# Kernel optimization log

Hardware: AMD Instinct MI355X
Metric: run time of the kernel (lower is better)

## Reference

```python
import jax, jax.numpy as jnp
import numpy as np

N = 40000          # nodes
E = 640000         # edges
D_IN, D_HID, D_EMB, D_OUT = 128, 128, 64, 2


def glorot(key, shape):
    lim = np.sqrt(6.0 / (shape[0] + shape[1]))
    return jax.random.uniform(key, shape, jnp.float32, -lim, lim)


def setup_inputs() -> dict:
    key = jax.random.key(0)
    ks = jax.random.split(key, 8)
    x = jax.random.normal(ks[0], (N, D_IN), jnp.float32)
    edge_index = jax.random.randint(ks[1], (2, E), 0, N, dtype=jnp.int64)
    # GCNConv weights stored as [in, out]; biases zero-init per PyG default
    W1 = glorot(ks[2], (D_IN, D_HID));  b1 = jnp.zeros((D_HID,), jnp.float32)
    W2 = glorot(ks[3], (D_HID, D_HID)); b2 = jnp.zeros((D_HID,), jnp.float32)
    W3 = glorot(ks[4], (D_HID, D_EMB)); b3 = jnp.zeros((D_EMB,), jnp.float32)
    Wout = glorot(ks[5], (D_EMB, D_OUT)); bout = jnp.zeros((D_OUT,), jnp.float32)
    return {"x": x, "edge_index": edge_index,
            "W1": W1, "b1": b1, "W2": W2, "b2": b2,
            "W3": W3, "b3": b3, "Wout": Wout, "bout": bout}


def _gcn_norm(edge_index, n):
    # add self loops, compute symmetric normalization d^-1/2[src] * d^-1/2[dst]
    loop = jnp.arange(n, dtype=edge_index.dtype)
    src = jnp.concatenate([edge_index[0], loop])
    dst = jnp.concatenate([edge_index[1], loop])
    deg = jax.ops.segment_sum(jnp.ones_like(dst, dtype=jnp.float32), dst,
                              num_segments=n)
    dinv = jax.lax.rsqrt(deg)                      # deg >= 1 due to self-loops
    dinv = jnp.where(jnp.isinf(dinv), 0.0, dinv)
    return src, dst, dinv[src] * dinv[dst]


def gcn_conv(x, src, dst, norm, W, b):
    h = x @ W                                      # [N, out]
    msg = h[src] * norm[:, None]                   # gather + scale  [E+N, out]
    return jax.ops.segment_sum(msg, dst, num_segments=x.shape[0]) + b


def reference(x, edge_index, W1, b1, W2, b2, W3, b3, Wout, bout):
    n = x.shape[0]
    src, dst, norm = _gcn_norm(edge_index, n)      # cached=True: computed once
    h = jax.nn.relu(gcn_conv(x, src, dst, norm, W1, b1))   # dropout is identity in eval
    h = jax.nn.relu(gcn_conv(h, src, dst, norm, W2, b2))
    h = gcn_conv(h, src, dst, norm, W3, b3)
    out = h @ Wout + bout
    return (out, h)
```

## Files before the change

### kernel.cpp

```cpp
#include <hip/hip_runtime.h>
#include <hip/hip_bf16.h>

#define NN 40000
#define NE 640000

typedef unsigned int u32;
typedef unsigned short u16;
typedef __attribute__((ext_vector_type(8))) short bf16x8;
typedef __attribute__((ext_vector_type(4))) float f32x4;

__device__ float g_wf[512];
__device__ u16   g_wp[40960];
__device__ int   g_flags[4];
__device__ int   g_cnt[NN];
__device__ int   g_cur[NN];
__device__ int   g_rowptr[NN + 1];
__device__ float g_dinv[NN];
__device__ int   g_csrc[NE];
__device__ int   g_bsum[64];
__device__ u16   g_ha[(size_t)NN * 128];
__device__ u16   g_hb[(size_t)NN * 128];

#define OFF_B1 0
#define OFF_B2 128
#define OFF_B3 256
#define OFF_WO 320
#define OFF_BO 448
#define WP_W1 0
#define WP_W2 16384
#define WP_W3 32768

__device__ __forceinline__ float b2f(u16 v){ return __uint_as_float(((u32)v) << 16); }
__device__ __forceinline__ float blo(u32 u){ return __uint_as_float(u << 16); }
__device__ __forceinline__ float bhi(u32 u){ return __uint_as_float(u & 0xffff0000u); }
__device__ __forceinline__ u32 f2bf(float f){
  u32 u = __float_as_uint(f);
  return (u + 0x7fffu + ((u >> 16) & 1u)) >> 16;
}
__device__ __forceinline__ int clampi(int v, int lo, int hi){ return v < lo ? lo : (v > hi ? hi : v); }
__device__ __forceinline__ u16 ldbf(const void* p, int idx){
  return g_flags[0] ? (u16)f2bf(((const float*)p)[idx]) : ((const u16*)p)[idx];
}
__device__ __forceinline__ float ldf(const void* p, int idx){
  return g_flags[0] ? ((const float*)p)[idx] : b2f(((const u16*)p)[idx]);
}

__global__ __launch_bounds__(256) void k_detect(const u16* __restrict__ xf, const int* __restrict__ ei){
  __shared__ int c1, c2;
  if (threadIdx.x == 0){ c1 = 0; c2 = 0; }
  __syncthreads();
  int l1 = 0, l2 = 0;
  for (int i = threadIdx.x; i < 4096; i += 256){
    u16 v = xf[2 * i];
    int e = (v >> 7) & 0xff;
    if (v == 0 || (e >= 100 && e <= 140)) l1++;
    if (ei[2 * i + 1] == 0) l2++;
  }
  atomicAdd(&c1, l1); atomicAdd(&c2, l2);
  __syncthreads();
  if (threadIdx.x == 0){
    g_flags[0] = (c1 < 2048) ? 1 : 0;
    g_flags[1] = (c2 > 2048) ? 2 : 1;
  }
}

__global__ __launch_bounds__(256) void k_prep(const void* xin, const void* w1, const void* b1,
                                              const void* w2, const void* b2, const void* w3,
                                              const void* b3, const void* wo, const void* bo){
  int T = (int)blockIdx.x * 256 + (int)threadIdx.x;
  if (T < 640000){
    if (g_flags[0]){
      const float4* p = (const float4*)xin + (size_t)T * 2;
      float4 a = p[0], b = p[1];
      uint4 o;
      o.x = f2bf(a.x) | (f2bf(a.y) << 16);
      o.y = f2bf(a.z) | (f2bf(a.w) << 16);
      o.z = f2bf(b.x) | (f2bf(b.y) << 16);
      o.w = f2bf(b.z) | (f2bf(b.w) << 16);
      ((uint4*)g_ha)[T] = o;
    } else {
      ((uint4*)g_ha)[T] = ((const uint4*)xin)[T];
    }
  } else if (T < 680960){
    int local = T - 640000;
    int J, dstbase, l; const void* src;
    if (local < 16384){ J = 128; src = w1; dstbase = WP_W1; l = local; }
    else if (local < 32768){ J = 128; src = w2; dstbase = WP_W2; l = local - 16384; }
    else { J = 64; src = w3; dstbase = WP_W3; l = local - 32768; }
    int chunk = l >> 9, within = l & 511;
    int nbw = J / 16;
    int kb = chunk / nbw, nb = chunk % nbw;
    int lane = within >> 3, j = within & 7;
    int q = lane >> 4, n = lane & 15;
    int k = kb * 32 + q * 8 + j;
    int col = nb * 16 + n;
    g_wp[dstbase + l] = ldbf(src, k * J + col);
  } else if (T < 681410){
    int l = T - 680960;
    if (l < 128)      g_wf[OFF_B1 + l] = ldf(b1, l);
    else if (l < 256) g_wf[OFF_B2 + l - 128] = ldf(b2, l - 128);
    else if (l < 320) g_wf[OFF_B3 + l - 256] = ldf(b3, l - 256);
    else if (l < 448) g_wf[OFF_WO + l - 320] = ldf(wo, l - 320);
    else              g_wf[OFF_BO + l - 448] = ldf(bo, l - 448);
  } else if (T < 721410){
    g_cnt[T - 681410] = 0;
  } else if (T < 761450){
    g_cur[T - 721410] = 0;
  }
}

__global__ __launch_bounds__(256) void k_count(const int* __restrict__ ei){
  int e = blockIdx.x * 256 + threadIdx.x;
  if (e < NE){
    int strd = g_flags[1];
    int d = clampi(ei[(size_t)(NE + e) * strd], 0, NN - 1);
    atomicAdd(&g_cnt[d], 1);
  }
}

__global__ __launch_bounds__(1024) void k_scan1(){
  int t = (int)threadIdx.x;
  int b = (int)blockIdx.x;
  int i = b * 1024 + t;
  int v = (i < NN) ? g_cnt[i] : 0;
  int lane = t & 63, wv = t >> 6;
  int x = v;
#pragma unroll
  for (int ofs = 1; ofs < 64; ofs <<= 1){
    int y = __shfl_up(x, ofs, 64);
    if (lane >= ofs) x += y;
  }
  __shared__ int wsum[16];
  if (lane == 63) wsum[wv] = x;
  __syncthreads();
  if (t < 16){
    int s = wsum[t];
#pragma unroll
    for (int ofs = 1; ofs < 16; ofs <<= 1){
      int y = __shfl_up(s, ofs, 64);
      if (t >= ofs) s += y;
    }
    wsum[t] = s;
  }
  __syncthreads();
  int pre = (wv == 0) ? 0 : wsum[wv - 1];
  int incl = x + pre;
  if (i < NN){
    g_rowptr[i] = incl - v;
    g_dinv[i] = rsqrtf((float)(v + 1));
  }
  if (t == 1023) g_bsum[b] = incl;
}

__global__ __launch_bounds__(1024) void k_scan3(){
  __shared__ int pre;
  int t = (int)threadIdx.x;
  if (t < 64){
    int v = (t < 40) ? g_bsum[t] : 0;
    int s = v;
#pragma unroll
    for (int ofs = 1; ofs < 64; ofs <<= 1){
      int y = __shfl_up(s, ofs, 64);
      if (t >= ofs) s += y;
    }
    if (t == (int)blockIdx.x) pre = s - v;
    if (blockIdx.x == 0 && t == 39) g_rowptr[NN] = s;
  }
  __syncthreads();
  int i = (int)blockIdx.x * 1024 + t;
  if (i < NN) g_rowptr[i] += pre;
}

__global__ __launch_bounds__(256) void k_fill(const int* __restrict__ ei){
  int part = (int)blockIdx.x & 7;
  int chunk = (int)blockIdx.x >> 3;
  int lo = part * 5000, hi = lo + 5000;
  int strd = g_flags[1];
  int tid = (int)threadIdx.x;
#pragma unroll
  for (int it = 0; it < 8; ++it){
    int e = chunk * 2048 + it * 256 + tid;
    if (e < NE){
      int d = clampi(ei[(size_t)(NE + e) * strd], 0, NN - 1);
      if (d >= lo && d < hi){
        int s = clampi(ei[(size_t)e * strd], 0, NN - 1);
        int pos = clampi(g_rowptr[d] + atomicAdd(&g_cur[d], 1), 0, NE - 1);
        g_csrc[pos] = s;
      }
    }
  }
}

template<int J>
__global__ __launch_bounds__(256) void k_gemm(int wpoff){
  constexpr int NB = J / 16;
  int tid = (int)threadIdx.x;
  int wave = tid >> 6, lane = tid & 63;
  int q = lane >> 4, n = lane & 15;
  int m0 = (int)blockIdx.x * 64 + wave * 16;
  f32x4 acc[NB];
#pragma unroll
  for (int nb = 0; nb < NB; ++nb) acc[nb] = (f32x4){0.f, 0.f, 0.f, 0.f};
  const u16* arow = g_ha + (size_t)(m0 + n) * 128 + q * 8;
#pragma unroll
  for (int kb = 0; kb < 4; ++kb){
    bf16x8 a = *(const bf16x8*)(arow + kb * 32);
    const u16* wbase = g_wp + wpoff + (kb * NB) * 512 + lane * 8;
#pragma unroll
    for (int nb = 0; nb < NB; ++nb){
      bf16x8 w = *(const bf16x8*)(wbase + nb * 512);
      acc[nb] = __builtin_amdgcn_mfma_f32_16x16x32_bf16(a, w, acc[nb], 0, 0, 0);
    }
  }
  u16* crow = g_hb + (size_t)(m0 + q * 4) * J + n;
#pragma unroll
  for (int r = 0; r < 4; ++r){
    float di = g_dinv[m0 + q * 4 + r];
#pragma unroll
    for (int nb = 0; nb < NB; ++nb)
      crow[(size_t)r * J + nb * 16] = (u16)f2bf(acc[nb][r] * di);
  }
}

#define ACC8(P) do { \
    a0 += blo((P).x); a1 += bhi((P).x); \
    a2 += blo((P).y); a3 += bhi((P).y); \
    a4 += blo((P).z); a5 += bhi((P).z); \
    a6 += blo((P).w); a7 += bhi((P).w); } while (0)

template<int J, bool RELU>
__global__ __launch_bounds__(256, 4) void k_agg(int boff, float* __restrict__ h3, float* __restrict__ outp){
  constexpr int LPR = J / 8;
  int gt = (int)blockIdx.x * 256 + (int)threadIdx.x;
  int wid = gt / LPR;
  int lane = (int)threadIdx.x & (LPR - 1);
  if (wid >= NN) return;
  int cc = lane * 8;
  const u16* __restrict__ hb = g_hb;
  float di = g_dinv[wid];
  int beg = g_rowptr[wid], end = g_rowptr[wid + 1];
  uint4 ps = *(const uint4*)(hb + (size_t)wid * J + cc);
  float a0 = 0.f, a1 = 0.f, a2 = 0.f, a3 = 0.f, a4 = 0.f, a5 = 0.f, a6 = 0.f, a7 = 0.f;
  for (int e = beg; e < end; e += 8){
    int s0, s1, s2, s3, s4, s5, s6, s7;
    {
      int last = end - 1;
#define LDS_IDX(T) clampi(g_csrc[(e + T < last) ? (e + T) : last], 0, NN - 1)
      s0 = LDS_IDX(0); s1 = LDS_IDX(1); s2 = LDS_IDX(2); s3 = LDS_IDX(3);
      s4 = LDS_IDX(4); s5 = LDS_IDX(5); s6 = LDS_IDX(6); s7 = LDS_IDX(7);
#undef LDS_IDX
    }
    uint4 p0 = *(const uint4*)(hb + (size_t)s0 * J + cc);
    uint4 p1 = *(const uint4*)(hb + (size_t)s1 * J + cc);
    uint4 p2 = *(const uint4*)(hb + (size_t)s2 * J + cc);
    uint4 p3 = *(const uint4*)(hb + (size_t)s3 * J + cc);
    uint4 p4 = *(const uint4*)(hb + (size_t)s4 * J + cc);
    uint4 p5 = *(const uint4*)(hb + (size_t)s5 * J + cc);
    uint4 p6 = *(const uint4*)(hb + (size_t)s6 * J + cc);
    uint4 p7 = *(const uint4*)(hb + (size_t)s7 * J + cc);
    int nv = end - e;
    ACC8(p0);
    if (nv > 1) ACC8(p1);
    if (nv > 2) ACC8(p2);
    if (nv > 3) ACC8(p3);
    if (nv > 4) ACC8(p4);
    if (nv > 5) ACC8(p5);
    if (nv > 6) ACC8(p6);
    if (nv > 7) ACC8(p7);
  }
  ACC8(ps);
  a0 = a0 * di + g_wf[boff + cc];
  a1 = a1 * di + g_wf[boff + cc + 1];
  a2 = a2 * di + g_wf[boff + cc + 2];
  a3 = a3 * di + g_wf[boff + cc + 3];
  a4 = a4 * di + g_wf[boff + cc + 4];
  a5 = a5 * di + g_wf[boff + cc + 5];
  a6 = a6 * di + g_wf[boff + cc + 6];
  a7 = a7 * di + g_wf[boff + cc + 7];
  if (RELU){
    a0 = fmaxf(a0, 0.f); a1 = fmaxf(a1, 0.f); a2 = fmaxf(a2, 0.f); a3 = fmaxf(a3, 0.f);
    a4 = fmaxf(a4, 0.f); a5 = fmaxf(a5, 0.f); a6 = fmaxf(a6, 0.f); a7 = fmaxf(a7, 0.f);
  }
  if (J == 128){
    uint4 o;
    o.x = f2bf(a0) | (f2bf(a1) << 16);
    o.y = f2bf(a2) | (f2bf(a3) << 16);
    o.z = f2bf(a4) | (f2bf(a5) << 16);
    o.w = f2bf(a6) | (f2bf(a7) << 16);
    *(uint4*)(g_ha + (size_t)wid * 128 + cc) = o;
  } else {
    *(float4*)(h3 + (size_t)wid * 64 + cc)     = make_float4(a0, a1, a2, a3);
    *(float4*)(h3 + (size_t)wid * 64 + cc + 4) = make_float4(a4, a5, a6, a7);
    float o0 = a0 * g_wf[OFF_WO + (cc + 0) * 2] + a1 * g_wf[OFF_WO + (cc + 1) * 2]
             + a2 * g_wf[OFF_WO + (cc + 2) * 2] + a3 * g_wf[OFF_WO + (cc + 3) * 2]
             + a4 * g_wf[OFF_WO + (cc + 4) * 2] + a5 * g_wf[OFF_WO + (cc + 5) * 2]
             + a6 * g_wf[OFF_WO + (cc + 6) * 2] + a7 * g_wf[OFF_WO + (cc + 7) * 2];
    float o1 = a0 * g_wf[OFF_WO + (cc + 0) * 2 + 1] + a1 * g_wf[OFF_WO + (cc + 1) * 2 + 1]
             + a2 * g_wf[OFF_WO + (cc + 2) * 2 + 1] + a3 * g_wf[OFF_WO + (cc + 3) * 2 + 1]
             + a4 * g_wf[OFF_WO + (cc + 4) * 2 + 1] + a5 * g_wf[OFF_WO + (cc + 5) * 2 + 1]
             + a6 * g_wf[OFF_WO + (cc + 6) * 2 + 1] + a7 * g_wf[OFF_WO + (cc + 7) * 2 + 1];
#pragma unroll
    for (int m = 1; m < 8; m <<= 1){
      o0 += __shfl_xor(o0, m, 64);
      o1 += __shfl_xor(o1, m, 64);
    }
    if (lane == 0){
      *(float2*)(outp + (size_t)wid * 2) =
        make_float2(o0 + g_wf[OFF_BO], o1 + g_wf[OFF_BO + 1]);
    }
  }
}

extern "C" void kernel_launch(void* const* d_in, const int* in_sizes, int n_in,
                              void* d_out, int out_size, void* d_ws, size_t ws_size,
                              hipStream_t stream){
  const int* ei = (const int*)d_in[1];
  float* out = (float*)d_out;
  float* h3  = out + (size_t)NN * 2;

  k_detect<<<1, 256, 0, stream>>>((const u16*)d_in[0], ei);
  k_prep<<<2975, 256, 0, stream>>>(d_in[0], d_in[2], d_in[3], d_in[4], d_in[5],
                                   d_in[6], d_in[7], d_in[8], d_in[9]);
  k_count<<<2500, 256, 0, stream>>>(ei);
  k_scan1<<<40, 1024, 0, stream>>>();
  k_scan3<<<40, 1024, 0, stream>>>();
  k_fill<<<2504, 256, 0, stream>>>(ei);

  k_gemm<128><<<625, 256, 0, stream>>>(WP_W1);
  k_agg<128, true><<<2500, 256, 0, stream>>>(OFF_B1, (float*)nullptr, (float*)nullptr);
  k_gemm<128><<<625, 256, 0, stream>>>(WP_W2);
  k_agg<128, true><<<2500, 256, 0, stream>>>(OFF_B2, (float*)nullptr, (float*)nullptr);
  k_gemm<64><<<625, 256, 0, stream>>>(WP_W3);
  k_agg<64, false><<<1250, 256, 0, stream>>>(OFF_B3, h3, out);
}
```

Before: 259.5 us.

## Inline dtype/stride detection into consumers and simplify CSR fill kernel

Removes the single-block detection kernel and instead has each wave in the prep, count and fill kernels detect input dtype and edge-index stride locally via a 64-lane ballot. This saves a kernel launch and its serialization. It also rewrites the fill kernel to handle one edge per thread over all destinations, rather than partitioning destinations into 8 ranges that each reread the edge list. The detection sample shrinks from 4096 to 64 values, which makes the heuristic less robust. The fill kernel's atomics are now spread across all nodes at once, which changes their contention and locality pattern.

```diff
diff --git a/kernel.cpp b/kernel.cpp
--- a/kernel.cpp
+++ b/kernel.cpp
@@ -11,7 +11,6 @@
 
 __device__ float g_wf[512];
 __device__ u16   g_wp[40960];
-__device__ int   g_flags[4];
 __device__ int   g_cnt[NN];
 __device__ int   g_cur[NN];
 __device__ int   g_rowptr[NN + 1];
@@ -38,38 +37,33 @@
   return (u + 0x7fffu + ((u >> 16) & 1u)) >> 16;
 }
 __device__ __forceinline__ int clampi(int v, int lo, int hi){ return v < lo ? lo : (v > hi ? hi : v); }
-__device__ __forceinline__ u16 ldbf(const void* p, int idx){
-  return g_flags[0] ? (u16)f2bf(((const float*)p)[idx]) : ((const u16*)p)[idx];
-}
-__device__ __forceinline__ float ldf(const void* p, int idx){
-  return g_flags[0] ? ((const float*)p)[idx] : b2f(((const u16*)p)[idx]);
-}
-
-__global__ __launch_bounds__(256) void k_detect(const u16* __restrict__ xf, const int* __restrict__ ei){
-  __shared__ int c1, c2;
-  if (threadIdx.x == 0){ c1 = 0; c2 = 0; }
-  __syncthreads();
-  int l1 = 0, l2 = 0;
-  for (int i = threadIdx.x; i < 4096; i += 256){
-    u16 v = xf[2 * i];
-    int e = (v >> 7) & 0xff;
-    if (v == 0 || (e >= 100 && e <= 140)) l1++;
-    if (ei[2 * i + 1] == 0) l2++;
-  }
-  atomicAdd(&c1, l1); atomicAdd(&c2, l2);
-  __syncthreads();
-  if (threadIdx.x == 0){
-    g_flags[0] = (c1 < 2048) ? 1 : 0;
-    g_flags[1] = (c2 > 2048) ? 2 : 1;
-  }
+__device__ __forceinline__ u16 ldbf(const void* p, int idx, int f32){
+  return f32 ? (u16)f2bf(((const float*)p)[idx]) : ((const u16*)p)[idx];
+}
+__device__ __forceinline__ float ldf(const void* p, int idx, int f32){
+  return f32 ? ((const float*)p)[idx] : b2f(((const u16*)p)[idx]);
+}
+
+__device__ __forceinline__ int detect_xf32(const u16* __restrict__ xf){
+  int i = ((int)threadIdx.x & 63) * 64;
+  u16 v = xf[2 * i];
+  int e = (v >> 7) & 0xff;
+  int pass = (v == 0 || (e >= 100 && e <= 140)) ? 1 : 0;
+  return (__popcll(__ballot(pass)) < 32) ? 1 : 0;
+}
+__device__ __forceinline__ int detect_estride(const int* __restrict__ ei){
+  int i = ((int)threadIdx.x & 63) * 64;
+  int pass = (ei[2 * i + 1] == 0) ? 1 : 0;
+  return (__popcll(__ballot(pass)) >= 32) ? 2 : 1;
 }
 
 __global__ __launch_bounds__(256) void k_prep(const void* xin, const void* w1, const void* b1,
                                               const void* w2, const void* b2, const void* w3,
                                               const void* b3, const void* wo, const void* bo){
+  int xf32 = detect_xf32((const u16*)xin);
   int T = (int)blockIdx.x * 256 + (int)threadIdx.x;
   if (T < 640000){
-    if (g_flags[0]){
+    if (xf32){
       const float4* p = (const float4*)xin + (size_t)T * 2;
       float4 a = p[0], b = p[1];
       uint4 o;
@@ -94,14 +88,14 @@
     int q = lane >> 4, n = lane & 15;
     int k = kb * 32 + q * 8 + j;
     int col = nb * 16 + n;
-    g_wp[dstbase + l] = ldbf(src, k * J + col);
+    g_wp[dstbase + l] = ldbf(src, k * J + col, xf32);
   } else if (T < 681410){
     int l = T - 680960;
-    if (l < 128)      g_wf[OFF_B1 + l] = ldf(b1, l);
-    else if (l < 256) g_wf[OFF_B2 + l - 128] = ldf(b2, l - 128);
-    else if (l < 320) g_wf[OFF_B3 + l - 256] = ldf(b3, l - 256);
-    else if (l < 448) g_wf[OFF_WO + l - 320] = ldf(wo, l - 320);
-    else              g_wf[OFF_BO + l - 448] = ldf(bo, l - 448);
+    if (l < 128)      g_wf[OFF_B1 + l] = ldf(b1, l, xf32);
+    else if (l < 256) g_wf[OFF_B2 + l - 128] = ldf(b2, l - 128, xf32);
+    else if (l < 320) g_wf[OFF_B3 + l - 256] = ldf(b3, l - 256, xf32);
+    else if (l < 448) g_wf[OFF_WO + l - 320] = ldf(wo, l - 320, xf32);
+    else              g_wf[OFF_BO + l - 448] = ldf(bo, l - 448, xf32);
   } else if (T < 721410){
     g_cnt[T - 681410] = 0;
   } else if (T < 761450){
@@ -110,9 +104,9 @@
 }
 
 __global__ __launch_bounds__(256) void k_count(const int* __restrict__ ei){
-  int e = blockIdx.x * 256 + threadIdx.x;
+  int strd = detect_estride(ei);
+  int e = (int)blockIdx.x * 256 + (int)threadIdx.x;
   if (e < NE){
-    int strd = g_flags[1];
     int d = clampi(ei[(size_t)(NE + e) * strd], 0, NN - 1);
     atomicAdd(&g_cnt[d], 1);
   }
@@ -172,22 +166,13 @@
 }
 
 __global__ __launch_bounds__(256) void k_fill(const int* __restrict__ ei){
-  int part = (int)blockIdx.x & 7;
-  int chunk = (int)blockIdx.x >> 3;
-  int lo = part * 5000, hi = lo + 5000;
-  int strd = g_flags[1];
-  int tid = (int)threadIdx.x;
-#pragma unroll
-  for (int it = 0; it < 8; ++it){
-    int e = chunk * 2048 + it * 256 + tid;
-    if (e < NE){
-      int d = clampi(ei[(size_t)(NE + e) * strd], 0, NN - 1);
-      if (d >= lo && d < hi){
-        int s = clampi(ei[(size_t)e * strd], 0, NN - 1);
-        int pos = clampi(g_rowptr[d] + atomicAdd(&g_cur[d], 1), 0, NE - 1);
-        g_csrc[pos] = s;
-      }
-    }
+  int strd = detect_estride(ei);
+  int e = (int)blockIdx.x * 256 + (int)threadIdx.x;
+  if (e < NE){
+    int d = clampi(ei[(size_t)(NE + e) * strd], 0, NN - 1);
+    int s = clampi(ei[(size_t)e * strd], 0, NN - 1);
+    int pos = clampi(g_rowptr[d] + atomicAdd(&g_cur[d], 1), 0, NE - 1);
+    g_csrc[pos] = s;
   }
 }
 
@@ -318,13 +303,12 @@
   float* out = (float*)d_out;
   float* h3  = out + (size_t)NN * 2;
 
-  k_detect<<<1, 256, 0, stream>>>((const u16*)d_in[0], ei);
   k_prep<<<2975, 256, 0, stream>>>(d_in[0], d_in[2], d_in[3], d_in[4], d_in[5],
                                    d_in[6], d_in[7], d_in[8], d_in[9]);
   k_count<<<2500, 256, 0, stream>>>(ei);
   k_scan1<<<40, 1024, 0, stream>>>();
   k_scan3<<<40, 1024, 0, stream>>>();
-  k_fill<<<2504, 256, 0, stream>>>(ei);
+  k_fill<<<2500, 256, 0, stream>>>(ei);
 
   k_gemm<128><<<625, 256, 0, stream>>>(WP_W1);
   k_agg<128, true><<<2500, 256, 0, stream>>>(OFF_B1, (float*)nullptr, (float*)nullptr);
```

New measurement: 253.2 us. -2.4%, faster.
